# Kernel optimization log

Hardware: AMD Instinct MI355X
Metric: run time of the kernel (lower is better)

Reference implementation:

```python
import jax, jax.numpy as jnp
import numpy as np

D_MODEL = 2048
NUM_HEADS = 32
NUM_KV_HEADS = 8
DIM_HEAD = D_MODEL // NUM_HEADS  # 64
REPS = NUM_HEADS // NUM_KV_HEADS  # 4
B, T = 2, 2048


def setup_inputs() -> dict:
    key = jax.random.key(0)
    k_x, k_q, k_k, k_v, k_o = jax.random.split(key, 5)
    s = 1.0 / np.sqrt(D_MODEL)
    return {
        "x": jax.random.normal(k_x, (B, T, D_MODEL), dtype=jnp.float32),
        "wq": jax.random.normal(k_q, (D_MODEL, NUM_HEADS * DIM_HEAD), dtype=jnp.float32) * s,
        "wk": jax.random.normal(k_k, (D_MODEL, NUM_KV_HEADS * DIM_HEAD), dtype=jnp.float32) * s,
        "wv": jax.random.normal(k_v, (D_MODEL, NUM_KV_HEADS * DIM_HEAD), dtype=jnp.float32) * s,
        "wo": jax.random.normal(k_o, (D_MODEL, D_MODEL), dtype=jnp.float32) * s,
    }


def reference(x, wq, wk, wv, wo):
    Bb, Tt, _ = x.shape
    q = (x @ wq).reshape(Bb, Tt, NUM_HEADS, DIM_HEAD)       # [B,T,H,dh]
    k = (x @ wk).reshape(Bb, Tt, NUM_KV_HEADS, DIM_HEAD)    # [B,T,Hkv,dh]
    v = (x @ wv).reshape(Bb, Tt, NUM_KV_HEADS, DIM_HEAD)
    # repeat_interleave KV heads to match Q heads
    k = jnp.repeat(k, REPS, axis=2)                          # [B,T,H,dh]
    v = jnp.repeat(v, REPS, axis=2)
    scale = 1.0 / np.sqrt(DIM_HEAD).astype(np.float32)
    scores = jnp.einsum('bqhd,bkhd->bhqk', q, k) * scale     # [B,H,T,T]
    causal = jnp.tril(jnp.ones((Tt, Tt), dtype=bool))
    scores = jnp.where(causal, scores, -jnp.inf)
    attn = jax.nn.softmax(scores, axis=-1)
    out = jnp.einsum('bhqk,bkhd->bqhd', attn, v)             # [B,T,H,dh]
    out = out.reshape(Bb, Tt, NUM_HEADS * DIM_HEAD)
    return out @ wo
```

## Files before the change

### kernel.cpp

```cpp
#include <hip/hip_runtime.h>

typedef unsigned short u16;
typedef unsigned int u32;
typedef unsigned long long u64;

typedef __bf16 bf16x8 __attribute__((ext_vector_type(8)));
typedef float f32x4 __attribute__((ext_vector_type(4)));
typedef u16 u16x4 __attribute__((ext_vector_type(4)));

__device__ __forceinline__ u16 f2bf(float f) {
  u32 u = __builtin_bit_cast(u32, f);
  u += 0x7fffu + ((u >> 16) & 1u);
  return (u16)(u >> 16);
}

__device__ __forceinline__ u32 packbf2(float a, float b) {
  __bf16 x = (__bf16)a, y = (__bf16)b;
  return (u32)__builtin_bit_cast(u16, x) | ((u32)__builtin_bit_cast(u16, y) << 16);
}

__device__ __forceinline__ float fexp2(float x) {
#if __has_builtin(__builtin_amdgcn_exp2f)
  return __builtin_amdgcn_exp2f(x);
#else
  return exp2f(x);
#endif
}

__device__ __forceinline__ void gload_lds16(const void* g, void* lds) {
  __builtin_amdgcn_global_load_lds(
      (const __attribute__((address_space(1))) void*)g,
      (__attribute__((address_space(3))) void*)lds, 16, 0, 0);
}

#define QSCALE 0.18033688011112043f

__global__ __launch_bounds__(256) void cast_f32_bf16(
    const float* __restrict__ in, u16* __restrict__ out, int n4) {
  int i = (blockIdx.x * 256 + threadIdx.x) * 4;
  float4 v = *reinterpret_cast<const float4*>(in + i);
  u16x4 o;
  o[0] = f2bf(v.x); o[1] = f2bf(v.y); o[2] = f2bf(v.z); o[3] = f2bf(v.w);
  *reinterpret_cast<u16x4*>(out + i) = o;
}

__global__ __launch_bounds__(256) void transpose_cast_all(
    const float* __restrict__ wq, const float* __restrict__ wk,
    const float* __restrict__ wv, const float* __restrict__ wo,
    u16* __restrict__ wqT, u16* __restrict__ wkT,
    u16* __restrict__ wvT, u16* __restrict__ woT) {
  constexpr int K = 2048;
  const float* w_;
  u16* wt;
  int N;
  switch (blockIdx.z) {
    case 0: w_ = wq; wt = wqT; N = 2048; break;
    case 1: w_ = wo; wt = woT; N = 2048; break;
    case 2: w_ = wk; wt = wkT; N = 512; break;
    default: w_ = wv; wt = wvT; N = 512; break;
  }
  int bx = blockIdx.x * 32;
  if (bx >= N) return;
  int by = blockIdx.y * 32;
  __shared__ float tile[32][33];
  int tx = threadIdx.x & 31, ty = threadIdx.x >> 5;
#pragma unroll
  for (int i = 0; i < 32; i += 8)
    tile[ty + i][tx] = w_[(size_t)(by + ty + i) * N + bx + tx];
  __syncthreads();
#pragma unroll
  for (int i = 0; i < 32; i += 8)
    wt[(size_t)(bx + ty + i) * K + by + tx] = f2bf(tile[tx][ty + i]);
}

__global__ __launch_bounds__(256) void transpose_u16(
    const u16* __restrict__ in, u16* __restrict__ out) {
  __shared__ u16 tile[32][33];
  int bx = blockIdx.x * 32;
  int by = blockIdx.y * 32;
  int bz = blockIdx.z;
  int tx = threadIdx.x & 31, ty = threadIdx.x >> 5;
#pragma unroll
  for (int i = 0; i < 32; i += 8)
    tile[ty + i][tx] = in[((size_t)bz * 2048 + bx + ty + i) * 512 + by + tx];
  __syncthreads();
#pragma unroll
  for (int i = 0; i < 32; i += 8)
    out[((size_t)bz * 512 + by + ty + i) * 2048 + bx + tx] = tile[tx][ty + i];
}

template <int MODE>
__global__ __launch_bounds__(512, 2) void gemm256(
    const u16* __restrict__ A, const u16* __restrict__ BT,
    float* __restrict__ Cf, u16* __restrict__ Cb, u16* __restrict__ Cb2,
    u16* __restrict__ Cb3, int M, int N) {
  constexpr int K = 2048, NT = 32;
  __shared__ __align__(16) u16 Ab[2][256 * 64];
  __shared__ __align__(16) u16 Bb[2][256 * 64];
  const int t = threadIdx.x;
  const int lane = t & 63;
  const int w = t >> 6;
  const int wm = w >> 2, wn = w & 3;
  const int l15 = lane & 15, l4 = lane >> 4;

  const int nwg = gridDim.x * gridDim.y;
  const int bid = blockIdx.y * gridDim.x + blockIdx.x;
  const int wg = (bid & 7) * (nwg >> 3) + (bid >> 3);
  const int brow = (wg / gridDim.x) * 256;
  const int bcol = (wg % gridDim.x) * 256;

  const int r0 = t >> 3;
  const int gc = ((t & 7) ^ (r0 & 7)) * 8;
  auto stageA = [&](int q, int h, int kt) {
    const u16* src = A + (size_t)(brow + h * 128 + r0) * K + kt * 64 + gc;
    u16* dst = &Ab[q][(h * 128 + r0) * 64 + (t & 7) * 8];
    gload_lds16(src, dst);
    gload_lds16(src + (size_t)64 * K, dst + 64 * 64);
  };
  auto stageB = [&](int q, int h, int kt) {
    const u16* src = BT + (size_t)(bcol + h * 128 + r0) * K + kt * 64 + gc;
    u16* dst = &Bb[q][(h * 128 + r0) * 64 + (t & 7) * 8];
    gload_lds16(src, dst);
    gload_lds16(src + (size_t)64 * K, dst + 64 * 64);
  };

  f32x4 acc[8][4];
#pragma unroll
  for (int mi = 0; mi < 8; mi++)
#pragma unroll
    for (int n = 0; n < 4; n++)
#pragma unroll
      for (int r = 0; r < 4; r++) acc[mi][n][r] = 0.f;

  stageA(0, 0, 0); stageA(0, 1, 0);
  stageB(0, 0, 0); stageB(0, 1, 0);
  stageA(1, 0, 1); stageA(1, 1, 1);
  asm volatile("s_waitcnt vmcnt(4)" ::: "memory");
  __builtin_amdgcn_sched_barrier(0);
  __builtin_amdgcn_s_barrier();

  for (int kt = 0; kt < NT; ++kt) {
    const int q = kt & 1;
    const u16* Al = Ab[q];
    const u16* Bl = Bb[q];
    bf16x8 af[8][2], bf[4][2];

#pragma unroll
    for (int m = 0; m < 4; ++m) {
      int row = wm * 128 + m * 16 + l15;
#pragma unroll
      for (int ks = 0; ks < 2; ++ks)
        af[m][ks] = *reinterpret_cast<const bf16x8*>(
            &Al[row * 64 + (((ks * 4 + l4) ^ (row & 7)) * 8)]);
    }
#pragma unroll
    for (int n = 0; n < 2; ++n) {
      int row = wn * 64 + n * 16 + l15;
#pragma unroll
      for (int ks = 0; ks < 2; ++ks)
        bf[n][ks] = *reinterpret_cast<const bf16x8*>(
            &Bl[row * 64 + (((ks * 4 + l4) ^ (row & 7)) * 8)]);
    }
    if (kt + 1 < NT) stageB(q ^ 1, 0, kt + 1);
    __builtin_amdgcn_s_barrier();
    __builtin_amdgcn_s_setprio(1);
#pragma unroll
    for (int ks = 0; ks < 2; ++ks)
#pragma unroll
      for (int m = 0; m < 4; ++m)
#pragma unroll
        for (int n = 0; n < 2; ++n)
          acc[m][n] = __builtin_amdgcn_mfma_f32_16x16x32_bf16(
              af[m][ks], bf[n][ks], acc[m][n], 0, 0, 0);
    __builtin_amdgcn_s_setprio(0);
    __builtin_amdgcn_s_barrier();

#pragma unroll
    for (int m = 4; m < 8; ++m) {
      int row = wm * 128 + m * 16 + l15;
#pragma unroll
      for (int ks = 0; ks < 2; ++ks)
        af[m][ks] = *reinterpret_cast<const bf16x8*>(
            &Al[row * 64 + (((ks * 4 + l4) ^ (row & 7)) * 8)]);
    }
#pragma unroll
    for (int n = 2; n < 4; ++n) {
      int row = wn * 64 + n * 16 + l15;
#pragma unroll
      for (int ks = 0; ks < 2; ++ks)
        bf[n][ks] = *reinterpret_cast<const bf16x8*>(
            &Bl[row * 64 + (((ks * 4 + l4) ^ (row & 7)) * 8)]);
    }
    if (kt + 1 < NT) stageB(q ^ 1, 1, kt + 1);
    __builtin_amdgcn_s_barrier();
    __builtin_amdgcn_s_setprio(1);
#pragma unroll
    for (int ks = 0; ks < 2; ++ks)
#pragma unroll
      for (int m = 0; m < 4; ++m)
#pragma unroll
        for (int n = 2; n < 4; ++n)
          acc[m][n] = __builtin_amdgcn_mfma_f32_16x16x32_bf16(
              af[m][ks], bf[n][ks], acc[m][n], 0, 0, 0);
    __builtin_amdgcn_s_setprio(0);
    __builtin_amdgcn_s_barrier();

    if (kt + 2 < NT) stageA(q, 0, kt + 2);
    __builtin_amdgcn_s_barrier();
    __builtin_amdgcn_s_setprio(1);
#pragma unroll
    for (int ks = 0; ks < 2; ++ks)
#pragma unroll
      for (int m = 4; m < 8; ++m)
#pragma unroll
        for (int n = 0; n < 2; ++n)
          acc[m][n] = __builtin_amdgcn_mfma_f32_16x16x32_bf16(
              af[m][ks], bf[n][ks], acc[m][n], 0, 0, 0);
    __builtin_amdgcn_s_setprio(0);
    __builtin_amdgcn_s_barrier();

    if (kt + 2 < NT) stageA(q, 1, kt + 2);
    __builtin_amdgcn_s_barrier();
    __builtin_amdgcn_s_setprio(1);
#pragma unroll
    for (int ks = 0; ks < 2; ++ks)
#pragma unroll
      for (int m = 4; m < 8; ++m)
#pragma unroll
        for (int n = 2; n < 4; ++n)
          acc[m][n] = __builtin_amdgcn_mfma_f32_16x16x32_bf16(
              af[m][ks], bf[n][ks], acc[m][n], 0, 0, 0);
    __builtin_amdgcn_s_setprio(0);
    if (kt + 2 < NT) {
      asm volatile("s_waitcnt vmcnt(4)" ::: "memory");
    } else {
      asm volatile("s_waitcnt vmcnt(0)" ::: "memory");
    }
    __builtin_amdgcn_sched_barrier(0);
    __builtin_amdgcn_s_barrier();
  }

#pragma unroll
  for (int mi = 0; mi < 8; ++mi) {
    int grow0 = brow + wm * 128 + mi * 16 + l4 * 4;
#pragma unroll
    for (int n = 0; n < 4; ++n) {
      int gcol = bcol + wn * 64 + n * 16 + l15;
#pragma unroll
      for (int r = 0; r < 4; ++r) {
        float v = acc[mi][n][r];
        if (MODE == 1) {
          Cf[(size_t)(grow0 + r) * N + gcol] = v;
        } else {
          if (bcol < 2048)
            Cb[(size_t)(grow0 + r) * 2048 + gcol] = f2bf(v * QSCALE);
          else if (bcol < 2560)
            Cb2[(size_t)(grow0 + r) * 512 + (gcol - 2048)] = f2bf(v);
          else
            Cb3[(size_t)(grow0 + r) * 512 + (gcol - 2560)] = f2bf(v);
        }
      }
    }
  }
}

template <int MODE>
__global__ __launch_bounds__(256) void gemm_bt(
    const u16* __restrict__ A, const u16* __restrict__ BT,
    float* __restrict__ Cf, u16* __restrict__ Cb, u16* __restrict__ Cb2,
    u16* __restrict__ Cb3, int M, int N) {
  constexpr int K = 2048;
  __shared__ __align__(16) u16 As[128 * 64];
  __shared__ __align__(16) u16 Bs[128 * 64];
  const int t = threadIdx.x;
  const int lane = t & 63;
  const int w = t >> 6;
  const int wr = w >> 1, wc = w & 1;
  const int l15 = lane & 15;
  const int l4 = lane >> 4;

  const int nwg = gridDim.x * gridDim.y;
  const int bid = blockIdx.y * gridDim.x + blockIdx.x;
  const int wg = (bid & 7) * (nwg >> 3) + (bid >> 3);
  const int brow = (wg / gridDim.x) * 128;
  const int bcol = (wg % gridDim.x) * 128;

  f32x4 acc[4][4];
#pragma unroll
  for (int m = 0; m < 4; m++)
#pragma unroll
    for (int n = 0; n < 4; n++)
#pragma unroll
      for (int r = 0; r < 4; r++) acc[m][n][r] = 0.f;

  const int r0 = t >> 3;
  const int gcs = ((t & 7) ^ (r0 & 7)) * 8;
  const u16* pa = A + (size_t)(brow + r0) * K + gcs;
  const u16* pb = BT + (size_t)(bcol + r0) * K + gcs;
  u16* const la = &As[t * 8];
  u16* const lb = &Bs[t * 8];

  for (int kk = 0; kk < K; kk += 64) {
#pragma unroll
    for (int c = 0; c < 4; ++c) {
      gload_lds16(pa + (size_t)c * 32 * K, la + c * 2048);
      gload_lds16(pb + (size_t)c * 32 * K, lb + c * 2048);
    }
    pa += 64;
    pb += 64;
    __syncthreads();
#pragma unroll
    for (int ks2 = 0; ks2 < 2; ++ks2) {
      bf16x8 a[4], b[4];
#pragma unroll
      for (int m = 0; m < 4; m++) {
        int row = wr * 64 + m * 16 + l15;
        a[m] = *reinterpret_cast<const bf16x8*>(
            &As[row * 64 + (((ks2 * 4 + l4) ^ (row & 7)) * 8)]);
      }
#pragma unroll
      for (int n = 0; n < 4; n++) {
        int row = wc * 64 + n * 16 + l15;
        b[n] = *reinterpret_cast<const bf16x8*>(
            &Bs[row * 64 + (((ks2 * 4 + l4) ^ (row & 7)) * 8)]);
      }
#pragma unroll
      for (int m = 0; m < 4; m++)
#pragma unroll
        for (int n = 0; n < 4; n++)
          acc[m][n] = __builtin_amdgcn_mfma_f32_16x16x32_bf16(a[m], b[n], acc[m][n], 0, 0, 0);
    }
    __syncthreads();
  }

#pragma unroll
  for (int m = 0; m < 4; m++) {
    int grow0 = brow + wr * 64 + m * 16 + l4 * 4;
#pragma unroll
    for (int n = 0; n < 4; n++) {
      int gcol = bcol + wc * 64 + n * 16 + l15;
#pragma unroll
      for (int r = 0; r < 4; r++) {
        if (MODE == 1) {
          Cf[(size_t)(grow0 + r) * N + gcol] = acc[m][n][r];
        } else {
          if (bcol < 2048)
            Cb[(size_t)(grow0 + r) * 2048 + gcol] = f2bf(acc[m][n][r] * QSCALE);
          else if (bcol < 2560)
            Cb2[(size_t)(grow0 + r) * 512 + (gcol - 2048)] = f2bf(acc[m][n][r]);
          else
            Cb3[(size_t)(grow0 + r) * 512 + (gcol - 2560)] = f2bf(acc[m][n][r]);
        }
      }
    }
  }
}

__global__ __launch_bounds__(256, 4) void attn_kernel(
    const u16* __restrict__ Qb, const u16* __restrict__ Kb,
    const u16* __restrict__ VT, u16* __restrict__ Ob) {
  const int jj = blockIdx.x;
  const int h = blockIdx.y, b = blockIdx.z;
  const int kvh = h >> 2;
  const int t = threadIdx.x;
  const int lane = t & 63;
  const int w = t >> 6;
  const int q15 = lane & 15, g = lane >> 4;

  __shared__ __align__(16) u16 Ks[2][64 * 64];
  __shared__ __align__(16) u16 Vs[2][64 * 64];
  __shared__ __align__(16) u32 Pu[4][16 * 32];

  const size_t Krow0 = (size_t)b * 2048;
  const size_t Vrow0 = ((size_t)b * 8 + kvh) * 64;

  auto stage = [&](int buf, int kvbase) {
#pragma unroll
    for (int c = 0; c < 2; ++c) {
      int chunk = c * 256 + t;
      int row = chunk >> 3, gg = chunk & 7;
      int gcs = (gg ^ (row & 7)) * 8;
      gload_lds16(&Kb[(Krow0 + kvbase + row) * 512 + kvh * 64 + gcs],
                  &Ks[buf][chunk * 8]);
      gload_lds16(&VT[(Vrow0 + row) * 2048 + kvbase + gcs],
                  &Vs[buf][chunk * 8]);
    }
  };

  const int swzB = (q15 & 7) << 3;
  const int swzP = (q15 & 7) << 2;
  u32* const pw = &Pu[w][0];
  const int nA = 32 - jj;
  const int nsteps = 33;
  auto kvb_of = [&](int ss) { return ((ss < nA) ? ss : ss - nA) << 6; };

  stage(0, 0);
  __syncthreads();
  int cur = 0;
  int ss = 0;

#pragma unroll
  for (int ph = 0; ph < 2; ++ph) {
    const int qt = ph ? jj : 31 - jj;
    const int nkv = qt + 1;
    const int wq0 = qt * 64 + w * 16;

    bf16x8 qf[2];
    {
      const u16* q0 = &Qb[((size_t)b * 2048 + wq0 + q15) * 2048 + h * 64 + g * 8];
      qf[0] = *reinterpret_cast<const bf16x8*>(q0);
      qf[1] = *reinterpret_cast<const bf16x8*>(q0 + 32);
    }

    f32x4 oo[4];
#pragma unroll
    for (int c = 0; c < 4; c++)
#pragma unroll
      for (int r = 0; r < 4; r++) oo[c][r] = 0.f;
    float mr = -1e30f, lr = 0.f;

    for (int kv = 0; kv < nkv; ++kv, ++ss) {
      const int kvbase = kv << 6;
      if (ss + 1 < nsteps) stage(cur ^ 1, kvb_of(ss + 1));

      f32x4 s[4];
#pragma unroll
      for (int c = 0; c < 4; c++)
#pragma unroll
        for (int r = 0; r < 4; r++) s[c][r] = 0.f;
      __builtin_amdgcn_s_setprio(1);
#pragma unroll
      for (int ks = 0; ks < 2; ++ks) {
        const int kcol = (ks * 32 + g * 8) ^ swzB;
#pragma unroll
        for (int c = 0; c < 4; c++) {
          bf16x8 kb = *reinterpret_cast<const bf16x8*>(
              &Ks[cur][(c * 16 + q15) * 64 + kcol]);
          s[c] = __builtin_amdgcn_mfma_f32_16x16x32_bf16(kb, qf[ks], s[c], 0, 0, 0);
        }
      }
      __builtin_amdgcn_s_setprio(0);

      if (kv == qt) {
        const int qg = wq0 + q15;
#pragma unroll
        for (int c = 0; c < 4; c++)
#pragma unroll
          for (int r = 0; r < 4; r++)
            if (kvbase + c * 16 + g * 4 + r > qg) s[c][r] = -1e30f;
      }

      float mx0 = fmaxf(fmaxf(s[0][0], s[0][1]), fmaxf(s[0][2], s[0][3]));
      float mx1 = fmaxf(fmaxf(s[1][0], s[1][1]), fmaxf(s[1][2], s[1][3]));
      float mx2 = fmaxf(fmaxf(s[2][0], s[2][1]), fmaxf(s[2][2], s[2][3]));
      float mx3 = fmaxf(fmaxf(s[3][0], s[3][1]), fmaxf(s[3][2], s[3][3]));
      float mx = fmaxf(fmaxf(mx0, mx1), fmaxf(mx2, mx3));
      mx = fmaxf(mx, __shfl_xor(mx, 16));
      mx = fmaxf(mx, __shfl_xor(mx, 32));
      if (!__all(mx <= mr + 8.f)) {
        float mnew = fmaxf(mr, mx);
        float alpha = fexp2(mr - mnew);
        lr *= alpha;
#pragma unroll
        for (int c = 0; c < 4; c++)
#pragma unroll
          for (int r = 0; r < 4; r++) oo[c][r] *= alpha;
        mr = mnew;
      }
      float p[4][4];
      float rs = 0.f;
#pragma unroll
      for (int c = 0; c < 4; c++) {
        float t0 = fexp2(s[c][0] - mr);
        float t1 = fexp2(s[c][1] - mr);
        float t2 = fexp2(s[c][2] - mr);
        float t3 = fexp2(s[c][3] - mr);
        p[c][0] = t0; p[c][1] = t1; p[c][2] = t2; p[c][3] = t3;
        rs += (t0 + t1) + (t2 + t3);
      }
      rs += __shfl_xor(rs, 16);
      rs += __shfl_xor(rs, 32);
      lr += rs;
#pragma unroll
      for (int c = 0; c < 4; c++) {
        u64 wv = (u64)packbf2(p[c][0], p[c][1]) |
                 ((u64)packbf2(p[c][2], p[c][3]) << 32);
        *reinterpret_cast<u64*>(&pw[q15 * 32 + ((c * 8 + g * 2) ^ swzP)]) = wv;
      }
      bf16x8 pb[2];
#pragma unroll
      for (int ks = 0; ks < 2; ++ks)
        pb[ks] = *reinterpret_cast<const bf16x8*>(
            &pw[q15 * 32 + ((ks * 16 + g * 4) ^ swzP)]);

      __builtin_amdgcn_s_setprio(1);
#pragma unroll
      for (int ks = 0; ks < 2; ++ks) {
        const int vcol = (ks * 32 + g * 8) ^ swzB;
#pragma unroll
        for (int c2 = 0; c2 < 4; c2++) {
          bf16x8 vb = *reinterpret_cast<const bf16x8*>(
              &Vs[cur][(c2 * 16 + q15) * 64 + vcol]);
          oo[c2] = __builtin_amdgcn_mfma_f32_16x16x32_bf16(vb, pb[ks], oo[c2], 0, 0, 0);
        }
      }
      __builtin_amdgcn_s_setprio(0);

      __syncthreads();
      cur ^= 1;
    }

    const int qq = lane >> 2, cl = lane & 3;
    const int swq = (qq & 7) << 2;
    {
      float rcp = 1.0f / lr;
#pragma unroll
      for (int c2 = 0; c2 < 4; c2++) {
        u64 wv = (u64)packbf2(oo[c2][0] * rcp, oo[c2][1] * rcp) |
                 ((u64)packbf2(oo[c2][2] * rcp, oo[c2][3] * rcp) << 32);
        *reinterpret_cast<u64*>(&pw[q15 * 32 + ((c2 * 8 + g * 2) ^ swzP)]) = wv;
      }
      uint4 d0 = *reinterpret_cast<const uint4*>(&pw[qq * 32 + ((cl * 4) ^ swq)]);
      uint4 d1 = *reinterpret_cast<const uint4*>(&pw[qq * 32 + ((cl * 4 + 16) ^ swq)]);
      u32* og = (u32*)Ob + ((size_t)b * 2048 + wq0 + qq) * 1024 + h * 32;
      *reinterpret_cast<uint4*>(&og[cl * 4]) = d0;
      *reinterpret_cast<uint4*>(&og[cl * 4 + 16]) = d1;
    }
  }
}

extern "C" void kernel_launch(void* const* d_in, const int* in_sizes, int n_in,
                              void* d_out, int out_size, void* d_ws, size_t ws_size,
                              hipStream_t stream) {
  const float* x = (const float*)d_in[0];
  const float* wq = (const float*)d_in[1];
  const float* wk = (const float*)d_in[2];
  const float* wv = (const float*)d_in[3];
  const float* wo = (const float*)d_in[4];
  float* out = (float*)d_out;

  char* p = (char*)d_ws;
  u16* xb = (u16*)p;   p += (size_t)4096 * 2048 * 2;
  u16* wqT = (u16*)p;  p += (size_t)2048 * 2048 * 2;
  u16* wkT = (u16*)p;  p += (size_t)512 * 2048 * 2;
  u16* wvT = (u16*)p;  p += (size_t)512 * 2048 * 2;
  u16* woT = (u16*)p;  p += (size_t)2048 * 2048 * 2;
  u16* Qb = (u16*)p;   p += (size_t)4096 * 2048 * 2;
  u16* Kb = (u16*)p;   p += (size_t)4096 * 512 * 2;
  u16* Vb = (u16*)p;   p += (size_t)4096 * 512 * 2;
  u16* VTb = (u16*)p;  p += (size_t)2 * 512 * 2048 * 2;
  u16* attn = xb;

  cast_f32_bf16<<<8192, 256, 0, stream>>>(x, xb, 4096 * 2048);
  transpose_cast_all<<<dim3(64, 64, 4), 256, 0, stream>>>(
      wq, wk, wv, wo, wqT, wkT, wvT, woT);

  gemm256<3><<<dim3(3072 / 256, 4096 / 256), 512, 0, stream>>>(
      xb, wqT, nullptr, Qb, Kb, Vb, 4096, 3072);

  transpose_u16<<<dim3(2048 / 32, 512 / 32, 2), 256, 0, stream>>>(Vb, VTb);

  attn_kernel<<<dim3(16, 32, 2), 256, 0, stream>>>(Qb, Kb, VTb, attn);

  gemm_bt<1><<<dim3(2048 / 128, 4096 / 128), 256, 0, stream>>>(
      attn, woT, out, nullptr, nullptr, nullptr, 4096, 2048);
}
```

Before: 198.7 us.

## Fuse V transpose into QKV epilogue, pipeline output GEMM, simplify attention staging

The QKV GEMM epilogue now writes V directly in transposed layout with packed 8-byte stores, so the separate transpose kernel and the intermediate V buffer go away. The output projection moves from a simple single-buffered 128x128 GEMM to a 256x128 double-buffered, phase-interleaved kernel with barriers and priority hints, similar to the QKV GEMM. Attention K/V staging precomputes base pointers and advances them incrementally instead of recomputing addresses each step. The transposed V stores are strided across rows, which may coalesce less well than the old row-major writes.

```diff
diff --git a/kernel.cpp b/kernel.cpp
--- a/kernel.cpp
+++ b/kernel.cpp
@@ -73,22 +73,6 @@
     wt[(size_t)(bx + ty + i) * K + by + tx] = f2bf(tile[tx][ty + i]);
 }
 
-__global__ __launch_bounds__(256) void transpose_u16(
-    const u16* __restrict__ in, u16* __restrict__ out) {
-  __shared__ u16 tile[32][33];
-  int bx = blockIdx.x * 32;
-  int by = blockIdx.y * 32;
-  int bz = blockIdx.z;
-  int tx = threadIdx.x & 31, ty = threadIdx.x >> 5;
-#pragma unroll
-  for (int i = 0; i < 32; i += 8)
-    tile[ty + i][tx] = in[((size_t)bz * 2048 + bx + ty + i) * 512 + by + tx];
-  __syncthreads();
-#pragma unroll
-  for (int i = 0; i < 32; i += 8)
-    out[((size_t)bz * 512 + by + ty + i) * 2048 + bx + tx] = tile[tx][ty + i];
-}
-
 template <int MODE>
 __global__ __launch_bounds__(512, 2) void gemm256(
     const u16* __restrict__ A, const u16* __restrict__ BT,
@@ -246,45 +230,61 @@
 #pragma unroll
     for (int n = 0; n < 4; ++n) {
       int gcol = bcol + wn * 64 + n * 16 + l15;
-#pragma unroll
-      for (int r = 0; r < 4; ++r) {
-        float v = acc[mi][n][r];
-        if (MODE == 1) {
-          Cf[(size_t)(grow0 + r) * N + gcol] = v;
-        } else {
-          if (bcol < 2048)
-            Cb[(size_t)(grow0 + r) * 2048 + gcol] = f2bf(v * QSCALE);
-          else if (bcol < 2560)
-            Cb2[(size_t)(grow0 + r) * 512 + (gcol - 2048)] = f2bf(v);
-          else
-            Cb3[(size_t)(grow0 + r) * 512 + (gcol - 2560)] = f2bf(v);
-        }
+      if (MODE == 1) {
+#pragma unroll
+        for (int r = 0; r < 4; ++r)
+          Cf[(size_t)(grow0 + r) * N + gcol] = acc[mi][n][r];
+      } else if (bcol < 2048) {
+#pragma unroll
+        for (int r = 0; r < 4; ++r)
+          Cb[(size_t)(grow0 + r) * 2048 + gcol] = f2bf(acc[mi][n][r] * QSCALE);
+      } else if (bcol < 2560) {
+#pragma unroll
+        for (int r = 0; r < 4; ++r)
+          Cb2[(size_t)(grow0 + r) * 512 + (gcol - 2048)] = f2bf(acc[mi][n][r]);
+      } else {
+        int col = gcol - 2560;
+        int bb = grow0 >> 11, tt = grow0 & 2047;
+        u64 wv = (u64)packbf2(acc[mi][n][0], acc[mi][n][1]) |
+                 ((u64)packbf2(acc[mi][n][2], acc[mi][n][3]) << 32);
+        *reinterpret_cast<u64*>(&Cb3[((size_t)(bb * 512 + col)) * 2048 + tt]) = wv;
       }
     }
   }
 }
 
-template <int MODE>
-__global__ __launch_bounds__(256) void gemm_bt(
+__global__ __launch_bounds__(512, 2) void gemm256n(
     const u16* __restrict__ A, const u16* __restrict__ BT,
-    float* __restrict__ Cf, u16* __restrict__ Cb, u16* __restrict__ Cb2,
-    u16* __restrict__ Cb3, int M, int N) {
-  constexpr int K = 2048;
-  __shared__ __align__(16) u16 As[128 * 64];
-  __shared__ __align__(16) u16 Bs[128 * 64];
+    float* __restrict__ Cf, int M, int N) {
+  constexpr int K = 2048, NT = 32;
+  __shared__ __align__(16) u16 Ab[2][256 * 64];
+  __shared__ __align__(16) u16 Bb[2][128 * 64];
   const int t = threadIdx.x;
   const int lane = t & 63;
   const int w = t >> 6;
-  const int wr = w >> 1, wc = w & 1;
-  const int l15 = lane & 15;
-  const int l4 = lane >> 4;
+  const int wm = w >> 1, wn = w & 1;
+  const int l15 = lane & 15, l4 = lane >> 4;
 
   const int nwg = gridDim.x * gridDim.y;
   const int bid = blockIdx.y * gridDim.x + blockIdx.x;
   const int wg = (bid & 7) * (nwg >> 3) + (bid >> 3);
-  const int brow = (wg / gridDim.x) * 128;
+  const int brow = (wg / gridDim.x) * 256;
   const int bcol = (wg % gridDim.x) * 128;
 
+  const int r0 = t >> 3;
+  const int gc = ((t & 7) ^ (r0 & 7)) * 8;
+  auto stageA = [&](int q, int h, int kt) {
+    const u16* src = A + (size_t)(brow + h * 128 + r0) * K + kt * 64 + gc;
+    u16* dst = &Ab[q][(h * 128 + r0) * 64 + (t & 7) * 8];
+    gload_lds16(src, dst);
+    gload_lds16(src + (size_t)64 * K, dst + 64 * 64);
+  };
+  auto stageB = [&](int q, int h, int kt) {
+    const u16* src = BT + (size_t)(bcol + h * 64 + r0) * K + kt * 64 + gc;
+    u16* dst = &Bb[q][(h * 64 + r0) * 64 + (t & 7) * 8];
+    gload_lds16(src, dst);
+  };
+
   f32x4 acc[4][4];
 #pragma unroll
   for (int m = 0; m < 4; m++)
@@ -293,65 +293,123 @@
 #pragma unroll
       for (int r = 0; r < 4; r++) acc[m][n][r] = 0.f;
 
-  const int r0 = t >> 3;
-  const int gcs = ((t & 7) ^ (r0 & 7)) * 8;
-  const u16* pa = A + (size_t)(brow + r0) * K + gcs;
-  const u16* pb = BT + (size_t)(bcol + r0) * K + gcs;
-  u16* const la = &As[t * 8];
-  u16* const lb = &Bs[t * 8];
-
-  for (int kk = 0; kk < K; kk += 64) {
-#pragma unroll
-    for (int c = 0; c < 4; ++c) {
-      gload_lds16(pa + (size_t)c * 32 * K, la + c * 2048);
-      gload_lds16(pb + (size_t)c * 32 * K, lb + c * 2048);
-    }
-    pa += 64;
-    pb += 64;
-    __syncthreads();
-#pragma unroll
-    for (int ks2 = 0; ks2 < 2; ++ks2) {
-      bf16x8 a[4], b[4];
-#pragma unroll
-      for (int m = 0; m < 4; m++) {
-        int row = wr * 64 + m * 16 + l15;
-        a[m] = *reinterpret_cast<const bf16x8*>(
-            &As[row * 64 + (((ks2 * 4 + l4) ^ (row & 7)) * 8)]);
-      }
-#pragma unroll
-      for (int n = 0; n < 4; n++) {
-        int row = wc * 64 + n * 16 + l15;
-        b[n] = *reinterpret_cast<const bf16x8*>(
-            &Bs[row * 64 + (((ks2 * 4 + l4) ^ (row & 7)) * 8)]);
-      }
-#pragma unroll
-      for (int m = 0; m < 4; m++)
-#pragma unroll
-        for (int n = 0; n < 4; n++)
-          acc[m][n] = __builtin_amdgcn_mfma_f32_16x16x32_bf16(a[m], b[n], acc[m][n], 0, 0, 0);
-    }
-    __syncthreads();
+  stageA(0, 0, 0); stageA(0, 1, 0);
+  stageB(0, 0, 0); stageB(0, 1, 0);
+  stageA(1, 0, 1); stageA(1, 1, 1);
+  asm volatile("s_waitcnt vmcnt(4)" ::: "memory");
+  __builtin_amdgcn_sched_barrier(0);
+  __builtin_amdgcn_s_barrier();
+
+  for (int kt = 0; kt < NT; ++kt) {
+    const int q = kt & 1;
+    const u16* Al = Ab[q];
+    const u16* Bl = Bb[q];
+    bf16x8 af[4][2], bf[4][2];
+
+#pragma unroll
+    for (int m = 0; m < 2; ++m) {
+      int row = wm * 64 + m * 16 + l15;
+#pragma unroll
+      for (int ks = 0; ks < 2; ++ks)
+        af[m][ks] = *reinterpret_cast<const bf16x8*>(
+            &Al[row * 64 + (((ks * 4 + l4) ^ (row & 7)) * 8)]);
+    }
+#pragma unroll
+    for (int n = 0; n < 2; ++n) {
+      int row = wn * 64 + n * 16 + l15;
+#pragma unroll
+      for (int ks = 0; ks < 2; ++ks)
+        bf[n][ks] = *reinterpret_cast<const bf16x8*>(
+            &Bl[row * 64 + (((ks * 4 + l4) ^ (row & 7)) * 8)]);
+    }
+    if (kt + 1 < NT) stageB(q ^ 1, 0, kt + 1);
+    __builtin_amdgcn_s_barrier();
+    __builtin_amdgcn_s_setprio(1);
+#pragma unroll
+    for (int ks = 0; ks < 2; ++ks)
+#pragma unroll
+      for (int m = 0; m < 2; ++m)
+#pragma unroll
+        for (int n = 0; n < 2; ++n)
+          acc[m][n] = __builtin_amdgcn_mfma_f32_16x16x32_bf16(
+              af[m][ks], bf[n][ks], acc[m][n], 0, 0, 0);
+    __builtin_amdgcn_s_setprio(0);
+    __builtin_amdgcn_s_barrier();
+
+#pragma unroll
+    for (int m = 2; m < 4; ++m) {
+      int row = wm * 64 + m * 16 + l15;
+#pragma unroll
+      for (int ks = 0; ks < 2; ++ks)
+        af[m][ks] = *reinterpret_cast<const bf16x8*>(
+            &Al[row * 64 + (((ks * 4 + l4) ^ (row & 7)) * 8)]);
+    }
+#pragma unroll
+    for (int n = 2; n < 4; ++n) {
+      int row = wn * 64 + n * 16 + l15;
+#pragma unroll
+      for (int ks = 0; ks < 2; ++ks)
+        bf[n][ks] = *reinterpret_cast<const bf16x8*>(
+            &Bl[row * 64 + (((ks * 4 + l4) ^ (row & 7)) * 8)]);
+    }
+    if (kt + 1 < NT) stageB(q ^ 1, 1, kt + 1);
+    __builtin_amdgcn_s_barrier();
+    __builtin_amdgcn_s_setprio(1);
+#pragma unroll
+    for (int ks = 0; ks < 2; ++ks)
+#pragma unroll
+      for (int m = 0; m < 2; ++m)
+#pragma unroll
+        for (int n = 2; n < 4; ++n)
+          acc[m][n] = __builtin_amdgcn_mfma_f32_16x16x32_bf16(
+              af[m][ks], bf[n][ks], acc[m][n], 0, 0, 0);
+    __builtin_amdgcn_s_setprio(0);
+    __builtin_amdgcn_s_barrier();
+
+    if (kt + 2 < NT) stageA(q, 0, kt + 2);
+    __builtin_amdgcn_s_barrier();
+    __builtin_amdgcn_s_setprio(1);
+#pragma unroll
+    for (int ks = 0; ks < 2; ++ks)
+#pragma unroll
+      for (int m = 2; m < 4; ++m)
+#pragma unroll
+        for (int n = 0; n < 2; ++n)
+          acc[m][n] = __builtin_amdgcn_mfma_f32_16x16x32_bf16(
+              af[m][ks], bf[n][ks], acc[m][n], 0, 0, 0);
+    __builtin_amdgcn_s_setprio(0);
+    __builtin_amdgcn_s_barrier();
+
+    if (kt + 2 < NT) stageA(q, 1, kt + 2);
+    __builtin_amdgcn_s_barrier();
+    __builtin_amdgcn_s_setprio(1);
+#pragma unroll
+    for (int ks = 0; ks < 2; ++ks)
+#pragma unroll
+      for (int m = 2; m < 4; ++m)
+#pragma unroll
+        for (int n = 2; n < 4; ++n)
+          acc[m][n] = __builtin_amdgcn_mfma_f32_16x16x32_bf16(
+              af[m][ks], bf[n][ks], acc[m][n], 0, 0, 0);
+    __builtin_amdgcn_s_setprio(0);
+    if (kt + 2 < NT) {
+      asm volatile("s_waitcnt vmcnt(4)" ::: "memory");
+    } else {
+      asm volatile("s_waitcnt vmcnt(0)" ::: "memory");
+    }
+    __builtin_amdgcn_sched_barrier(0);
+    __builtin_amdgcn_s_barrier();
   }
 
 #pragma unroll
-  for (int m = 0; m < 4; m++) {
-    int grow0 = brow + wr * 64 + m * 16 + l4 * 4;
-#pragma unroll
-    for (int n = 0; n < 4; n++) {
-      int gcol = bcol + wc * 64 + n * 16 + l15;
-#pragma unroll
-      for (int r = 0; r < 4; r++) {
-        if (MODE == 1) {
-          Cf[(size_t)(grow0 + r) * N + gcol] = acc[m][n][r];
-        } else {
-          if (bcol < 2048)
-            Cb[(size_t)(grow0 + r) * 2048 + gcol] = f2bf(acc[m][n][r] * QSCALE);
-          else if (bcol < 2560)
-            Cb2[(size_t)(grow0 + r) * 512 + (gcol - 2048)] = f2bf(acc[m][n][r]);
-          else
-            Cb3[(size_t)(grow0 + r) * 512 + (gcol - 2560)] = f2bf(acc[m][n][r]);
-        }
-      }
+  for (int m = 0; m < 4; ++m) {
+    int grow0 = brow + wm * 64 + m * 16 + l4 * 4;
+#pragma unroll
+    for (int n = 0; n < 4; ++n) {
+      int gcol = bcol + wn * 64 + n * 16 + l15;
+#pragma unroll
+      for (int r = 0; r < 4; ++r)
+        Cf[(size_t)(grow0 + r) * N + gcol] = acc[m][n][r];
     }
   }
 }
@@ -374,17 +432,24 @@
   const size_t Krow0 = (size_t)b * 2048;
   const size_t Vrow0 = ((size_t)b * 8 + kvh) * 64;
 
-  auto stage = [&](int buf, int kvbase) {
-#pragma unroll
-    for (int c = 0; c < 2; ++c) {
-      int chunk = c * 256 + t;
-      int row = chunk >> 3, gg = chunk & 7;
-      int gcs = (gg ^ (row & 7)) * 8;
-      gload_lds16(&Kb[(Krow0 + kvbase + row) * 512 + kvh * 64 + gcs],
-                  &Ks[buf][chunk * 8]);
-      gload_lds16(&VT[(Vrow0 + row) * 2048 + kvbase + gcs],
-                  &Vs[buf][chunk * 8]);
-    }
+  u16* const dk0 = &Ks[0][t * 8];
+  u16* const dk1 = &Ks[1][t * 8];
+  u16* const dv0 = &Vs[0][t * 8];
+  u16* const dv1 = &Vs[1][t * 8];
+  const int row0 = t >> 3;
+  const int gcs = ((t & 7) ^ (row0 & 7)) * 8;
+  const u16* const pk0 = Kb + (Krow0 + row0) * 512 + kvh * 64 + gcs;
+  const u16* const pv0 = VT + (Vrow0 + row0) * 2048 + gcs;
+  const u16* kp = pk0;
+  const u16* vp = pv0;
+
+  auto stage = [&](int buf, const u16* kpp, const u16* vpp) {
+    u16* dk = buf ? dk1 : dk0;
+    u16* dv = buf ? dv1 : dv0;
+    gload_lds16(kpp, dk);
+    gload_lds16(kpp + 32 * 512, dk + 2048);
+    gload_lds16(vpp, dv);
+    gload_lds16(vpp + 32 * 2048, dv + 2048);
   };
 
   const int swzB = (q15 & 7) << 3;
@@ -392,9 +457,8 @@
   u32* const pw = &Pu[w][0];
   const int nA = 32 - jj;
   const int nsteps = 33;
-  auto kvb_of = [&](int ss) { return ((ss < nA) ? ss : ss - nA) << 6; };
-
-  stage(0, 0);
+
+  stage(0, kp, vp);
   __syncthreads();
   int cur = 0;
   int ss = 0;
@@ -421,7 +485,16 @@
 
     for (int kv = 0; kv < nkv; ++kv, ++ss) {
       const int kvbase = kv << 6;
-      if (ss + 1 < nsteps) stage(cur ^ 1, kvb_of(ss + 1));
+      if (ss + 1 < nsteps) {
+        if (ss + 1 == nA) {
+          kp = pk0;
+          vp = pv0;
+        } else {
+          kp += 64 * 512;
+          vp += 64;
+        }
+        stage(cur ^ 1, kp, vp);
+      }
 
       f32x4 s[4];
 #pragma unroll
@@ -547,7 +620,6 @@
   u16* woT = (u16*)p;  p += (size_t)2048 * 2048 * 2;
   u16* Qb = (u16*)p;   p += (size_t)4096 * 2048 * 2;
   u16* Kb = (u16*)p;   p += (size_t)4096 * 512 * 2;
-  u16* Vb = (u16*)p;   p += (size_t)4096 * 512 * 2;
   u16* VTb = (u16*)p;  p += (size_t)2 * 512 * 2048 * 2;
   u16* attn = xb;
 
@@ -556,12 +628,10 @@
       wq, wk, wv, wo, wqT, wkT, wvT, woT);
 
   gemm256<3><<<dim3(3072 / 256, 4096 / 256), 512, 0, stream>>>(
-      xb, wqT, nullptr, Qb, Kb, Vb, 4096, 3072);
-
-  transpose_u16<<<dim3(2048 / 32, 512 / 32, 2), 256, 0, stream>>>(Vb, VTb);
+      xb, wqT, nullptr, Qb, Kb, VTb, 4096, 3072);
 
   attn_kernel<<<dim3(16, 32, 2), 256, 0, stream>>>(Qb, Kb, VTb, attn);
 
-  gemm_bt<1><<<dim3(2048 / 128, 4096 / 128), 256, 0, stream>>>(
-      attn, woT, out, nullptr, nullptr, nullptr, 4096, 2048);
-}
+  gemm256n<<<dim3(2048 / 128, 4096 / 256), 512, 0, stream>>>(
+      attn, woT, out, 4096, 2048);
+}
```

Result: faster. 193.9 us (-2.4%).
